# Kernel optimization log

Measured on AMD Instinct MI355X. Metric: run time of the kernel, lower is better.

The kernel has to match this reference:

```python
import jax, jax.numpy as jnp
import numpy as np

N = 256
M = 180


def _fft3_centered(u):
    # centered 3D FFT: shift so that frequency 0 is at index n//2
    return jnp.fft.fftshift(jnp.fft.fftn(jnp.fft.ifftshift(u)))


def _ifft2_centered(s):
    ax = (-2, -1)
    return jnp.fft.fftshift(jnp.fft.ifft2(jnp.fft.ifftshift(s, axes=ax), axes=ax), axes=ax)


def _trilinear(F, pos):
    """Sample complex 3D grid F (n,n,n) at fractional index positions pos (...,3).
    Points outside the grid contribute zero (frequencies beyond Nyquist)."""
    n = F.shape[0]
    p0f = jnp.floor(pos)
    f = pos - p0f                      # fractional part, in [0,1)
    p0 = p0f.astype(jnp.int32)
    acc = jnp.zeros(pos.shape[:-1], dtype=F.dtype)
    for dx in (0, 1):
        for dy in (0, 1):
            for dz in (0, 1):
                idx = p0 + jnp.array([dx, dy, dz], jnp.int32)
                w = ((f[..., 0] if dx else 1.0 - f[..., 0])
                     * (f[..., 1] if dy else 1.0 - f[..., 1])
                     * (f[..., 2] if dz else 1.0 - f[..., 2]))
                valid = jnp.all((idx >= 0) & (idx < n), axis=-1)
                idc = jnp.clip(idx, 0, n - 1)
                val = F[idc[..., 0], idc[..., 1], idc[..., 2]]  # irregular gather
                acc = acc + jnp.where(valid, w, 0.0) * val
    return acc


def _lamino_fwd(weight, theta, tilt):
    """NUFFT laminography forward projector (Fourier-slice formulation).
    weight: (n,n,n,2) real/imag volume; theta: (M,) angles; tilt: scalar.
    Returns (M,n,n,2) projections, matching tike's Lamino.fwd math: the 2D
    Fourier transform of each projection equals the 3D FT of the volume
    sampled on a plane tilted by `tilt` and rotated by `theta` about z."""
    n = weight.shape[0]
    u = jax.lax.complex(weight[..., 0], weight[..., 1])
    F = _fft3_centered(u)                                   # (n,n,n) complex64
    fr = ((jnp.arange(n) - n // 2) / n).astype(jnp.float32)  # [-0.5, 0.5)
    kv, ku = jnp.meshgrid(fr, fr, indexing='ij')            # detector freq grid
    ct, st = jnp.cos(theta), jnp.sin(theta)                 # (M,)
    cp_, sp = jnp.cos(tilt), jnp.sin(tilt)
    one = jnp.ones_like(ct)
    e_u = jnp.stack([ct, st, 0.0 * ct], -1)                 # (M,3) horizontal axis
    e_v = jnp.stack([-st * cp_, ct * cp_, sp * one], -1)    # (M,3) tilted axis
    # 3D non-uniform frequencies for every (angle, detector pixel): (M,n,n,3)
    k3 = ku[None, :, :, None] * e_u[:, None, None, :] + kv[None, :, :, None] * e_v[:, None, None, :]
    pos = k3 * n + n // 2                                   # fractional grid coords
    samples = _trilinear(F, pos)                            # (M,n,n) complex
    proj = _ifft2_centered(samples)                         # (M,n,n) complex
    return jnp.stack([proj.real, proj.imag], -1).astype(jnp.float32)


def setup_inputs() -> dict:
    key = jax.random.key(0)
    k1, k2 = jax.random.split(key)
    weight = jax.random.normal(k1, (N, N, N, 2), dtype=jnp.float32)
    theta = jax.random.uniform(k2, (M,), dtype=jnp.float32) * (2.0 * np.pi)
    tilt = jnp.float32(1.0)  # laminography tilt angle (rad); source default pi/2
    return {"weight": weight, "theta": theta, "tilt": tilt}


def reference(weight, theta, tilt):
    return _lamino_fwd(weight, theta, tilt)
```

## Files before the change

### kernel.cpp

```cpp
#include <hip/hip_runtime.h>
#include <math.h>


namespace {

__device__ __forceinline__ void fft16_reg(float (&re)[16], float (&im)[16],
                                          bool inv) {
  const float C16[8] = {1.0f, 0.92387953251128675613f, 0.70710678118654752440f,
                        0.38268343236508977173f, 0.0f, -0.38268343236508977173f,
                        -0.70710678118654752440f, -0.92387953251128675613f};
  const float S16[8] = {0.0f, 0.38268343236508977173f, 0.70710678118654752440f,
                        0.92387953251128675613f, 1.0f, 0.92387953251128675613f,
                        0.70710678118654752440f, 0.38268343236508977173f};
  #pragma unroll
  for (int s = 0; s < 4; s++) {
    const int h = 8 >> s;
    #pragma unroll
    for (int g = 0; g < (8 >> (3 - s)); g++) {
      #pragma unroll
      for (int p = 0; p < h; p++) {
        const int i = g * 2 * h + p;
        const int j = i + h;
        const float ar = re[i], ai = im[i], br = re[j], bi = im[j];
        re[i] = ar + br;
        im[i] = ai + bi;
        const float dr = ar - br, di = ai - bi;
        const int t = p << s;
        const float wr = C16[t];
        const float wi = inv ? S16[t] : -S16[t];
        re[j] = dr * wr - di * wi;
        im[j] = dr * wi + di * wr;
      }
    }
  }
}

template<int MODE, bool INV>
__global__ __launch_bounds__(256)
void fft_pass(const float2* __restrict__ in, float2* __restrict__ out) {
  __shared__ float2 zt[16 * 273];
  const int t  = threadIdx.x;
  const int tx = t & 15;
  const int ty = t >> 4;
  const int idA = (MODE == 0) ? tx : ty;
  const int lin = (MODE == 0) ? ty : tx;
  const int lineIdx = (int)blockIdx.x * 16 + lin;
  int base, stride;
  if (MODE == 0)      { base = lineIdx * 256;                            stride = 1;     }
  else if (MODE == 1) { base = (lineIdx >> 8) * 65536 + (lineIdx & 255); stride = 256;   }
  else                { base = lineIdx;                                  stride = 65536; }

  const int BR4[16] = {0, 8, 4, 12, 2, 10, 6, 14, 1, 9, 5, 13, 3, 11, 7, 15};

  float re[16], im[16];

  {
    const float s1 = (idA & 1) ? -1.0f : 1.0f;
    #pragma unroll
    for (int n2 = 0; n2 < 16; n2++) {
      const float2 v = in[base + (idA + 16 * n2) * stride];
      re[n2] = v.x * s1;
      im[n2] = v.y * s1;
    }
    fft16_reg(re, im, INV);
    const float TWO_PI = 6.28318530717958647692f;
    const float ang = (INV ? TWO_PI : -TWO_PI) * ((float)idA * (1.0f / 256.0f));
    float ss, cc;
    sincosf(ang, &ss, &cc);
    float wr = 1.0f, wi = 0.0f;
    #pragma unroll
    for (int k2 = 0; k2 < 16; k2++) {
      const float yr = re[BR4[k2]], yi = im[BR4[k2]];
      zt[lin * 273 + idA * 17 + k2] =
          make_float2(yr * wr - yi * wi, yr * wi + yi * wr);
      const float nwr = wr * cc - wi * ss;
      wi = wr * ss + wi * cc;
      wr = nwr;
    }
  }
  __syncthreads();
  {
    #pragma unroll
    for (int n1 = 0; n1 < 16; n1++) {
      const float2 z = zt[lin * 273 + n1 * 17 + idA];
      re[n1] = z.x;
      im[n1] = z.y;
    }
    fft16_reg(re, im, INV);
    const float sOut = ((idA & 1) ? -1.0f : 1.0f) * (INV ? (1.0f / 256.0f) : 1.0f);
    #pragma unroll
    for (int k1 = 0; k1 < 16; k1++) {
      out[base + (idA + 16 * k1) * stride] =
          make_float2(re[BR4[k1]] * sOut, im[BR4[k1]] * sOut);
    }
  }
}

__global__ __launch_bounds__(256)
void sample_kernel(const float2* __restrict__ F, float2* __restrict__ out,
                   const float* __restrict__ theta, const float* __restrict__ tiltp) {
  __shared__ float2 tile[16][18];
  const int m  = blockIdx.z;
  const int tx = threadIdx.x;
  const int ty = threadIdx.y;
  const int a = blockIdx.x * 16 + tx;
  const int b = blockIdx.y * 16 + ty;
  float th = theta[m];
  float st, ct;
  sincosf(th, &st, &ct);
  float tl = tiltp[0];
  float sp, cp;
  sincosf(tl, &sp, &cp);
  float bu = (float)(b - 128);
  float av = (float)(a - 128);
  float p0 = bu * ct + av * (-st * cp) + 128.0f;
  float p1 = bu * st + av * (ct * cp) + 128.0f;
  float p2 = av * sp + 128.0f;
  float f0 = floorf(p0), f1 = floorf(p1), f2 = floorf(p2);
  int x0 = (int)f0, y0 = (int)f1, z0 = (int)f2;
  float fx = p0 - f0, fy = p1 - f1, fz = p2 - f2;
  float accr = 0.0f, acci = 0.0f;
  #pragma unroll
  for (int dx = 0; dx < 2; dx++) {
    int x = x0 + dx;
    bool vx = (x >= 0) && (x < 256);
    int xc = min(max(x, 0), 255);
    float wx = dx ? fx : (1.0f - fx);
    #pragma unroll
    for (int dy = 0; dy < 2; dy++) {
      int y = y0 + dy;
      bool vy = vx && (y >= 0) && (y < 256);
      int yc = min(max(y, 0), 255);
      float wxy = wx * (dy ? fy : (1.0f - fy));
      int rowbase = (xc * 256 + yc) * 256;
      #pragma unroll
      for (int dz = 0; dz < 2; dz++) {
        int z = z0 + dz;
        bool v = vy && (z >= 0) && (z < 256);
        int zc = min(max(z, 0), 255);
        float w = v ? wxy * (dz ? fz : (1.0f - fz)) : 0.0f;
        float2 c = F[rowbase + zc];
        accr += w * c.x;
        acci += w * c.y;
      }
    }
  }
  tile[ty][tx] = make_float2(accr, acci);
  __syncthreads();
  const int oa = blockIdx.x * 16 + ty;
  const int ob = blockIdx.y * 16 + tx;
  out[((size_t)m * 256 + oa) * 256 + ob] = tile[tx][ty];
}

}

extern "C" void kernel_launch(void* const* d_in, const int* in_sizes, int n_in,
                              void* d_out, int out_size, void* d_ws, size_t ws_size,
                              hipStream_t stream) {
  const float2* w  = (const float2*)d_in[0];
  const float*  th = (const float*)d_in[1];
  const float*  tl = (const float*)d_in[2];
  float2* F    = (float2*)d_ws;
  float2* out2 = (float2*)d_out;

  fft_pass<0, false><<<4096, 256, 0, stream>>>(w, F);
  fft_pass<1, false><<<4096, 256, 0, stream>>>(F, F);
  fft_pass<2, false><<<4096, 256, 0, stream>>>(F, F);

  dim3 g(16, 16, 180), blk(16, 16);
  sample_kernel<<<g, blk, 0, stream>>>(F, out2, th, tl);

  fft_pass<0, true><<<2880, 256, 0, stream>>>(out2, out2);
  fft_pass<1, true><<<2880, 256, 0, stream>>>(out2, out2);
}
```

Measured before the change: 523.4 us.

## Fuse trilinear sampling with first inverse FFT pass along detector rows

The sampling kernel now has each block compute 16 detector columns across all 256 row positions for one angle. It feeds the gathered samples straight into a register/shared-memory radix-16x16 inverse FFT along that axis and writes the transformed lines. This removes one full write and read of the (M,n,n) complex sample array and one kernel launch. The z-weights are also hoisted per thread. The cost is more per-thread work and different gather locality, since each thread now loops over 16 b values.

```diff
diff --git a/kernel.cpp b/kernel.cpp
--- a/kernel.cpp
+++ b/kernel.cpp
@@ -3,6 +3,9 @@
 
 
 namespace {
+
+__device__ const int BR4[16] = {0, 8, 4, 12, 2, 10, 6, 14,
+                                1, 9, 5, 13, 3, 11, 7, 15};
 
 __device__ __forceinline__ void fft16_reg(float (&re)[16], float (&im)[16],
                                           bool inv) {
@@ -50,8 +53,6 @@
   else if (MODE == 1) { base = (lineIdx >> 8) * 65536 + (lineIdx & 255); stride = 256;   }
   else                { base = lineIdx;                                  stride = 65536; }
 
-  const int BR4[16] = {0, 8, 4, 12, 2, 10, 6, 14, 1, 9, 5, 13, 3, 11, 7, 15};
-
   float re[16], im[16];
 
   {
@@ -97,59 +98,106 @@
 }
 
 __global__ __launch_bounds__(256)
-void sample_kernel(const float2* __restrict__ F, float2* __restrict__ out,
-                   const float* __restrict__ theta, const float* __restrict__ tiltp) {
-  __shared__ float2 tile[16][18];
-  const int m  = blockIdx.z;
-  const int tx = threadIdx.x;
-  const int ty = threadIdx.y;
-  const int a = blockIdx.x * 16 + tx;
-  const int b = blockIdx.y * 16 + ty;
+void sample_ifftb(const float2* __restrict__ F, float2* __restrict__ out,
+                  const float* __restrict__ theta, const float* __restrict__ tiltp) {
+  __shared__ float2 zt[16 * 273];
+  const int t  = threadIdx.x;
+  const int tx = t & 15;
+  const int ty = t >> 4;
+  const int m  = blockIdx.y;
+  const int a  = blockIdx.x * 16 + tx;
+
   float th = theta[m];
   float st, ct;
   sincosf(th, &st, &ct);
   float tl = tiltp[0];
   float sp, cp;
   sincosf(tl, &sp, &cp);
-  float bu = (float)(b - 128);
-  float av = (float)(a - 128);
-  float p0 = bu * ct + av * (-st * cp) + 128.0f;
-  float p1 = bu * st + av * (ct * cp) + 128.0f;
-  float p2 = av * sp + 128.0f;
-  float f0 = floorf(p0), f1 = floorf(p1), f2 = floorf(p2);
-  int x0 = (int)f0, y0 = (int)f1, z0 = (int)f2;
-  float fx = p0 - f0, fy = p1 - f1, fz = p2 - f2;
-  float accr = 0.0f, acci = 0.0f;
+
+  const float av = (float)(a - 128);
+  const float p2 = av * sp + 128.0f;
+  const float f2 = floorf(p2);
+  const int   z0 = (int)f2;
+  const float fz = p2 - f2;
+  const int   z1 = z0 + 1;
+  const float wz0 = ((z0 >= 0) && (z0 < 256)) ? (1.0f - fz) : 0.0f;
+  const float wz1 = ((z1 >= 0) && (z1 < 256)) ? fz : 0.0f;
+  const int  zc0 = min(max(z0, 0), 255);
+  const int  zc1 = min(max(z1, 0), 255);
+  const float p0b = av * (-st * cp) + 128.0f;
+  const float p1b = av * (ct * cp) + 128.0f;
+
+  float re[16], im[16];
+  const float s1 = (ty & 1) ? -1.0f : 1.0f;
   #pragma unroll
-  for (int dx = 0; dx < 2; dx++) {
-    int x = x0 + dx;
-    bool vx = (x >= 0) && (x < 256);
-    int xc = min(max(x, 0), 255);
-    float wx = dx ? fx : (1.0f - fx);
-    #pragma unroll
-    for (int dy = 0; dy < 2; dy++) {
-      int y = y0 + dy;
-      bool vy = vx && (y >= 0) && (y < 256);
-      int yc = min(max(y, 0), 255);
-      float wxy = wx * (dy ? fy : (1.0f - fy));
-      int rowbase = (xc * 256 + yc) * 256;
+  for (int n2 = 0; n2 < 16; n2++) {
+    const int b = ty + 16 * n2;
+    const float bu = (float)(b - 128);
+    const float p0 = bu * ct + p0b;
+    const float p1 = bu * st + p1b;
+    const float f0 = floorf(p0), f1 = floorf(p1);
+    const int x0 = (int)f0, y0 = (int)f1;
+    const float fx = p0 - f0, fy = p1 - f1;
+    float accr = 0.0f, acci = 0.0f;
+    #pragma unroll
+    for (int dx = 0; dx < 2; dx++) {
+      const int x = x0 + dx;
+      const bool vx = (x >= 0) && (x < 256);
+      const int xc = min(max(x, 0), 255);
+      const float wx = dx ? fx : (1.0f - fx);
       #pragma unroll
-      for (int dz = 0; dz < 2; dz++) {
-        int z = z0 + dz;
-        bool v = vy && (z >= 0) && (z < 256);
-        int zc = min(max(z, 0), 255);
-        float w = v ? wxy * (dz ? fz : (1.0f - fz)) : 0.0f;
-        float2 c = F[rowbase + zc];
-        accr += w * c.x;
-        acci += w * c.y;
+      for (int dy = 0; dy < 2; dy++) {
+        const int y = y0 + dy;
+        const bool vy = vx && (y >= 0) && (y < 256);
+        const int yc = min(max(y, 0), 255);
+        const float wxy = vy ? wx * (dy ? fy : (1.0f - fy)) : 0.0f;
+        const int rowbase = (xc * 256 + yc) * 256;
+        const float2 c0 = F[rowbase + zc0];
+        const float2 c1 = F[rowbase + zc1];
+        const float w0 = wxy * wz0;
+        const float w1 = wxy * wz1;
+        accr += w0 * c0.x + w1 * c1.x;
+        acci += w0 * c0.y + w1 * c1.y;
       }
     }
-  }
-  tile[ty][tx] = make_float2(accr, acci);
+    re[n2] = accr * s1;
+    im[n2] = acci * s1;
+  }
+  fft16_reg(re, im, true);
+  {
+    const float TWO_PI = 6.28318530717958647692f;
+    const float ang = TWO_PI * ((float)ty * (1.0f / 256.0f));
+    float ss, cc;
+    sincosf(ang, &ss, &cc);
+    float wr = 1.0f, wi = 0.0f;
+    #pragma unroll
+    for (int k2 = 0; k2 < 16; k2++) {
+      const float yr = re[BR4[k2]], yi = im[BR4[k2]];
+      zt[tx * 273 + ty * 17 + k2] =
+          make_float2(yr * wr - yi * wi, yr * wi + yi * wr);
+      const float nwr = wr * cc - wi * ss;
+      wi = wr * ss + wi * cc;
+      wr = nwr;
+    }
+  }
   __syncthreads();
-  const int oa = blockIdx.x * 16 + ty;
-  const int ob = blockIdx.y * 16 + tx;
-  out[((size_t)m * 256 + oa) * 256 + ob] = tile[tx][ty];
+  {
+    #pragma unroll
+    for (int n1 = 0; n1 < 16; n1++) {
+      const float2 z = zt[ty * 273 + n1 * 17 + tx];
+      re[n1] = z.x;
+      im[n1] = z.y;
+    }
+    fft16_reg(re, im, true);
+    const float sOut = ((tx & 1) ? -1.0f : 1.0f) * (1.0f / 256.0f);
+    const int aB = blockIdx.x * 16 + ty;
+    const size_t base = ((size_t)m * 256 + aB) * 256;
+    #pragma unroll
+    for (int k1 = 0; k1 < 16; k1++) {
+      out[base + tx + 16 * k1] =
+          make_float2(re[BR4[k1]] * sOut, im[BR4[k1]] * sOut);
+    }
+  }
 }
 
 }
@@ -167,9 +215,8 @@
   fft_pass<1, false><<<4096, 256, 0, stream>>>(F, F);
   fft_pass<2, false><<<4096, 256, 0, stream>>>(F, F);
 
-  dim3 g(16, 16, 180), blk(16, 16);
-  sample_kernel<<<g, blk, 0, stream>>>(F, out2, th, tl);
-
-  fft_pass<0, true><<<2880, 256, 0, stream>>>(out2, out2);
+  dim3 g(16, 180);
+  sample_ifftb<<<g, 256, 0, stream>>>(F, out2, th, tl);
+
   fft_pass<1, true><<<2880, 256, 0, stream>>>(out2, out2);
 }
```

New measurement: 569.0 us. 1.09x slower.
